# Performance work log

Measured on AMD Instinct MI355X. Metric: run time of the kernel, lower is better.

## Reference

```python
import jax, jax.numpy as jnp
import numpy as np

B, S, H, NH, FF = 16, 1024, 768, 12, 3072
D = H // NH  # 64
EPS = 1e-12


def layer_norm(x, g, b):
    mu = jnp.mean(x, axis=-1, keepdims=True)
    var = jnp.mean(jnp.square(x - mu), axis=-1, keepdims=True)
    return (x - mu) * jax.lax.rsqrt(var + EPS) * g + b


def setup_inputs() -> dict:
    key = jax.random.key(0)
    ks = jax.random.split(key, 16)
    w = lambda k, shape: (jax.random.normal(k, shape, jnp.float32) * 0.02)
    return {
        "features": jax.random.normal(ks[0], (B, S, H), jnp.float32),
        "attention_mask": jnp.zeros((B, S), jnp.float32),  # additive mask
        "wq": w(ks[1], (H, H)), "bq": jnp.zeros((H,), jnp.float32),
        "wk": w(ks[2], (H, H)), "bk": jnp.zeros((H,), jnp.float32),
        "wv": w(ks[3], (H, H)), "bv": jnp.zeros((H,), jnp.float32),
        "wo": w(ks[4], (H, H)), "bo": jnp.zeros((H,), jnp.float32),
        "ln1_g": jnp.ones((H,), jnp.float32), "ln1_b": jnp.zeros((H,), jnp.float32),
        "w1": w(ks[5], (H, FF)), "b1": jnp.zeros((FF,), jnp.float32),
        "w2": w(ks[6], (FF, H)), "b2": jnp.zeros((H,), jnp.float32),
        "ln2_g": jnp.ones((H,), jnp.float32), "ln2_b": jnp.zeros((H,), jnp.float32),
        "wp": w(ks[7], (H, H)), "bp": jnp.zeros((H,), jnp.float32),
        "wm": w(ks[8], (H, 1)), "bm": jnp.zeros((1,), jnp.float32),
    }


def reference(features, attention_mask, wq, bq, wk, bk, wv, bv, wo, bo,
              ln1_g, ln1_b, w1, b1, w2, b2, ln2_g, ln2_b, wp, bp, wm, bm):
    mask = attention_mask[:, None, None, :]  # [B,1,1,S]

    def split_heads(x):  # [B,S,H] -> [B,NH,S,D]
        return x.reshape(B, S, NH, D).transpose(0, 2, 1, 3)

    q = split_heads(features @ wq + bq)
    k = split_heads(features @ wk + bk)
    v = split_heads(features @ wv + bv)

    scores = jnp.einsum("bhqd,bhkd->bhqk", q, k) / np.sqrt(D).astype(np.float32)
    probs = jax.nn.softmax(scores + mask, axis=-1)  # dropout is identity (eval)
    ctx = jnp.einsum("bhqk,bhkd->bhqd", probs, v)
    ctx = ctx.transpose(0, 2, 1, 3).reshape(B, S, H)

    attn_out = layer_norm(ctx @ wo + bo + features, ln1_g, ln1_b)
    ffn = jax.nn.gelu(attn_out @ w1 + b1, approximate=False) @ w2 + b2
    hidden = layer_norm(ffn + attn_out, ln2_g, ln2_b)

    pooled = jnp.tanh(hidden[:, 0] @ wp + bp)  # BertPooler on [CLS]
    cls = (pooled @ wm + bm).squeeze()  # [B]
    return cls
```

## Files before the change

### kernel.cpp

```cpp
#include <hip/hip_runtime.h>
#include <math.h>

namespace {

constexpr int B  = 16;
constexpr int S  = 1024;
constexpr int H  = 768;
constexpr int NH = 12;
constexpr int DH = 64;
constexpr int FF = 3072;
constexpr int KSPL = 16;
constexpr float EPS = 1e-12f;

__device__ __forceinline__ float waveReduceSum(float v) {
#pragma unroll
    for (int d = 1; d < 64; d <<= 1) v += __shfl_xor(v, d);
    return v;
}

__device__ __forceinline__ float blockReduceSum768(float v, float* red) {
    const int lane = threadIdx.x & 63;
    const int wid  = threadIdx.x >> 6;
    v = waveReduceSum(v);
    __syncthreads();
    if (lane == 0) red[wid] = v;
    __syncthreads();
    float s = 0.f;
#pragma unroll
    for (int w = 0; w < 12; ++w) s += red[w];
    return s;
}

template <int K, int ISPL, int N>
__global__ __launch_bounds__(256) void gemm_partial(
        const float* __restrict__ A, int lda, int jtOfsA,
        const float* __restrict__ W, float* __restrict__ part) {
    constexpr int IR = K / ISPL;
    __shared__ float Asl[B * IR];
    const int jt  = blockIdx.x;
    const int sp  = blockIdx.y;
    const int i0  = sp * IR;
    const int tid = threadIdx.x;

    for (int e = tid; e < B * IR; e += 256) {
        const int b = e / IR, ii = e % IR;
        Asl[e] = A[(size_t)b * lda + (size_t)jt * jtOfsA + i0 + ii];
    }
    __syncthreads();

    const int jl = tid & 63;
    const int bg = tid >> 6;
    const int j  = jt * 64 + jl;
    const float* wp_ = W + (size_t)i0 * N + j;
    const float* a0 = Asl + (bg * 4 + 0) * IR;
    const float* a1 = Asl + (bg * 4 + 1) * IR;
    const float* a2 = Asl + (bg * 4 + 2) * IR;
    const float* a3 = Asl + (bg * 4 + 3) * IR;
    float acc0 = 0.f, acc1 = 0.f, acc2 = 0.f, acc3 = 0.f;
#pragma unroll
    for (int ii = 0; ii < IR; ++ii) {
        const float w = wp_[(size_t)ii * N];
        acc0 += w * a0[ii];
        acc1 += w * a1[ii];
        acc2 += w * a2[ii];
        acc3 += w * a3[ii];
    }
    float* pp = part + ((size_t)sp * B) * N + j;
    pp[(size_t)(bg * 4 + 0) * N] = acc0;
    pp[(size_t)(bg * 4 + 1) * N] = acc1;
    pp[(size_t)(bg * 4 + 2) * N] = acc2;
    pp[(size_t)(bg * 4 + 3) * N] = acc3;
}

template <int K, int ISPL, int N, int RED>
__global__ __launch_bounds__(256) void gemm_partial_red(
        const float* __restrict__ Ain, const float* __restrict__ bias,
        const float* __restrict__ W, float* __restrict__ part) {
    constexpr int IR = K / ISPL;
    __shared__ float Asl[B * IR];
    const int jt  = blockIdx.x;
    const int sp  = blockIdx.y;
    const int i0  = sp * IR;
    const int tid = threadIdx.x;

    for (int e = tid; e < B * IR; e += 256) {
        const int b = e / IR, ii = e % IR;
        float v = bias[i0 + ii];
#pragma unroll
        for (int sp2 = 0; sp2 < RED; ++sp2)
            v += Ain[((size_t)sp2 * B + b) * K + i0 + ii];
        Asl[e] = v;
    }
    __syncthreads();

    const int jl = tid & 63;
    const int bg = tid >> 6;
    const int j  = jt * 64 + jl;
    const float* wp_ = W + (size_t)i0 * N + j;
    const float* a0 = Asl + (bg * 4 + 0) * IR;
    const float* a1 = Asl + (bg * 4 + 1) * IR;
    const float* a2 = Asl + (bg * 4 + 2) * IR;
    const float* a3 = Asl + (bg * 4 + 3) * IR;
    float acc0 = 0.f, acc1 = 0.f, acc2 = 0.f, acc3 = 0.f;
#pragma unroll
    for (int ii = 0; ii < IR; ++ii) {
        const float w = wp_[(size_t)ii * N];
        acc0 += w * a0[ii];
        acc1 += w * a1[ii];
        acc2 += w * a2[ii];
        acc3 += w * a3[ii];
    }
    float* pp = part + ((size_t)sp * B) * N + j;
    pp[(size_t)(bg * 4 + 0) * N] = acc0;
    pp[(size_t)(bg * 4 + 1) * N] = acc1;
    pp[(size_t)(bg * 4 + 2) * N] = acc2;
    pp[(size_t)(bg * 4 + 3) * N] = acc3;
}

template <int K, int ISPL, int N, int RED>
__global__ __launch_bounds__(256) void gemm_partial_red_gelu(
        const float* __restrict__ Ain, const float* __restrict__ bias,
        const float* __restrict__ W, float* __restrict__ part) {
    constexpr int IR = K / ISPL;
    __shared__ float Asl[B * IR];
    const int jt  = blockIdx.x;
    const int sp  = blockIdx.y;
    const int i0  = sp * IR;
    const int tid = threadIdx.x;

    for (int e = tid; e < B * IR; e += 256) {
        const int b = e / IR, ii = e % IR;
        float v = bias[i0 + ii];
#pragma unroll
        for (int sp2 = 0; sp2 < RED; ++sp2)
            v += Ain[((size_t)sp2 * B + b) * K + i0 + ii];
        Asl[e] = 0.5f * v * (1.0f + erff(v * 0.70710678118654752440f));
    }
    __syncthreads();

    const int jl = tid & 63;
    const int bg = tid >> 6;
    const int j  = jt * 64 + jl;
    const float* wp_ = W + (size_t)i0 * N + j;
    const float* a0 = Asl + (bg * 4 + 0) * IR;
    const float* a1 = Asl + (bg * 4 + 1) * IR;
    const float* a2 = Asl + (bg * 4 + 2) * IR;
    const float* a3 = Asl + (bg * 4 + 3) * IR;
    float acc0 = 0.f, acc1 = 0.f, acc2 = 0.f, acc3 = 0.f;
#pragma unroll 32
    for (int ii = 0; ii < IR; ++ii) {
        const float w = wp_[(size_t)ii * N];
        acc0 += w * a0[ii];
        acc1 += w * a1[ii];
        acc2 += w * a2[ii];
        acc3 += w * a3[ii];
    }
    float* pp = part + ((size_t)sp * B) * N + j;
    pp[(size_t)(bg * 4 + 0) * N] = acc0;
    pp[(size_t)(bg * 4 + 1) * N] = acc1;
    pp[(size_t)(bg * 4 + 2) * N] = acc2;
    pp[(size_t)(bg * 4 + 3) * N] = acc3;
}

template <int ISPL>
__global__ __launch_bounds__(256) void gemm_xpart(
        const float* __restrict__ xpart, const float* __restrict__ W,
        float* __restrict__ part) {
    constexpr int IR = H / ISPL;
    __shared__ float Asl[B * IR];
    const int jt  = blockIdx.x;
    const int sp  = blockIdx.y;
    const int i0  = sp * IR;
    const int tid = threadIdx.x;

    for (int e = tid; e < B * IR; e += 256) {
        const int b = e / IR, ii = e % IR;
        float v = 0.f;
#pragma unroll
        for (int s2 = 0; s2 < KSPL; ++s2)
            v += xpart[(((size_t)(b * KSPL + s2)) * NH + jt) * H + i0 + ii];
        Asl[e] = v;
    }
    __syncthreads();

    const int jl = tid & 63;
    const int bg = tid >> 6;
    const int j  = jt * 64 + jl;
    const float* wp_ = W + (size_t)i0 * H + j;
    const float* a0 = Asl + (bg * 4 + 0) * IR;
    const float* a1 = Asl + (bg * 4 + 1) * IR;
    const float* a2 = Asl + (bg * 4 + 2) * IR;
    const float* a3 = Asl + (bg * 4 + 3) * IR;
    float acc0 = 0.f, acc1 = 0.f, acc2 = 0.f, acc3 = 0.f;
#pragma unroll
    for (int ii = 0; ii < IR; ++ii) {
        const float w = wp_[(size_t)ii * H];
        acc0 += w * a0[ii];
        acc1 += w * a1[ii];
        acc2 += w * a2[ii];
        acc3 += w * a3[ii];
    }
    float* pp = part + ((size_t)sp * B) * H + j;
    pp[(size_t)(bg * 4 + 0) * H] = acc0;
    pp[(size_t)(bg * 4 + 1) * H] = acc1;
    pp[(size_t)(bg * 4 + 2) * H] = acc2;
    pp[(size_t)(bg * 4 + 3) * H] = acc3;
}

__global__ __launch_bounds__(256) void u_kernel(
        const float* __restrict__ q0_part, const float* __restrict__ bq,
        const float* __restrict__ wk, const float* __restrict__ bk,
        float* __restrict__ u, float* __restrict__ constk) {
    const int b = blockIdx.x / NH, h = blockIdx.x % NH;
    __shared__ float qh[DH];
    const int tid = threadIdx.x;
    if (tid < DH) {
        float v = bq[h * DH + tid];
#pragma unroll
        for (int sp = 0; sp < 24; ++sp)
            v += q0_part[((size_t)sp * B + b) * H + h * DH + tid];
        qh[tid] = v;
    }
    __syncthreads();
    if (tid < DH) {
        float v = bk[h * DH + tid] * qh[tid];
        v = waveReduceSum(v);
        if (tid == 0) constk[b * NH + h] = v;
    }
    const int jj = tid & 3, iq = tid >> 2;
    const float4* qv = (const float4*)qh;
    float4 q4[4];
#pragma unroll
    for (int c = 0; c < 4; ++c) q4[c] = qv[jj * 4 + c];
#pragma unroll 4
    for (int ir = 0; ir < 12; ++ir) {
        const int i = ir * 64 + iq;
        const float4* wr = (const float4*)(wk + (size_t)i * H + h * DH);
        float s = 0.f;
#pragma unroll
        for (int c = 0; c < 4; ++c) {
            const float4 w = wr[jj * 4 + c];
            s += w.x * q4[c].x + w.y * q4[c].y + w.z * q4[c].z + w.w * q4[c].w;
        }
        s += __shfl_xor(s, 1);
        s += __shfl_xor(s, 2);
        if (jj == 0) u[((size_t)(b * NH + h)) * H + i] = s;
    }
}

__global__ __launch_bounds__(256, 2) void score_kernel(
        const float* __restrict__ x, const float* __restrict__ u,
        const float* __restrict__ constk, const float* __restrict__ mask,
        float* __restrict__ e_t, float* __restrict__ psum) {
    const int b  = blockIdx.x;
    const int kt = blockIdx.y;
    __shared__ __align__(16) float ul[NH * H];
    __shared__ float ck[NH];
    __shared__ float wsum[4][NH];
    const int tid = threadIdx.x;
    {
        const float4* ug = (const float4*)(u + (size_t)b * NH * H);
        float4* ul4 = (float4*)ul;
        for (int e = tid; e < NH * H / 4; e += 256) ul4[e] = ug[e];
        if (tid < NH) ck[tid] = constk[b * NH + tid];
    }
    __syncthreads();

    const int jj = tid & 15, kk = tid >> 4;
    const int k0 = kt * 32 + kk * 2;
    float4 xv0[12], xv1[12];
    {
        const float4* xr0 = (const float4*)(x + ((size_t)b * S + k0) * H);
        const float4* xr1 = (const float4*)(x + ((size_t)b * S + k0 + 1) * H);
#pragma unroll
        for (int t = 0; t < 12; ++t) { xv0[t] = xr0[jj + 16 * t]; xv1[t] = xr1[jj + 16 * t]; }
    }
    const float4* ul4 = (const float4*)ul;
    float acc0[NH], acc1[NH];
#pragma unroll
    for (int h = 0; h < NH; ++h) {
        float a0 = 0.f, a1 = 0.f;
#pragma unroll
        for (int t = 0; t < 12; ++t) {
            const float4 uv = ul4[h * 192 + jj + 16 * t];
            a0 += xv0[t].x * uv.x + xv0[t].y * uv.y + xv0[t].z * uv.z + xv0[t].w * uv.w;
            a1 += xv1[t].x * uv.x + xv1[t].y * uv.y + xv1[t].z * uv.z + xv1[t].w * uv.w;
        }
        acc0[h] = a0; acc1[h] = a1;
    }
#pragma unroll
    for (int h = 0; h < NH; ++h) {
#pragma unroll
        for (int d = 1; d < 16; d <<= 1) {
            acc0[h] += __shfl_xor(acc0[h], d);
            acc1[h] += __shfl_xor(acc1[h], d);
        }
    }
    const float mk0 = mask[b * S + k0];
    const float mk1 = mask[b * S + k0 + 1];
    float e0[NH], e1[NH], ps[NH];
#pragma unroll
    for (int h = 0; h < NH; ++h) {
        e0[h] = expf(acc0[h] * 0.125f + ck[h] + mk0);
        e1[h] = expf(acc1[h] * 0.125f + ck[h] + mk1);
        ps[h] = e0[h] + e1[h];
    }
    if (jj == 0) {
        float4* er0 = (float4*)(e_t + ((size_t)(b * S + k0)) * NH);
        float4* er1 = (float4*)(e_t + ((size_t)(b * S + k0 + 1)) * NH);
        er0[0] = make_float4(e0[0], e0[1], e0[2], e0[3]);
        er0[1] = make_float4(e0[4], e0[5], e0[6], e0[7]);
        er0[2] = make_float4(e0[8], e0[9], e0[10], e0[11]);
        er1[0] = make_float4(e1[0], e1[1], e1[2], e1[3]);
        er1[1] = make_float4(e1[4], e1[5], e1[6], e1[7]);
        er1[2] = make_float4(e1[8], e1[9], e1[10], e1[11]);
    }
#pragma unroll
    for (int h = 0; h < NH; ++h) {
        ps[h] += __shfl_xor(ps[h], 16);
        ps[h] += __shfl_xor(ps[h], 32);
    }
    const int wid = tid >> 6;
    if ((tid & 63) == 0) {
#pragma unroll
        for (int h = 0; h < NH; ++h) wsum[wid][h] = ps[h];
    }
    __syncthreads();
    if (tid < NH)
        psum[((size_t)(b * 32 + kt)) * NH + tid] =
            wsum[0][tid] + wsum[1][tid] + wsum[2][tid] + wsum[3][tid];
}

__global__ __launch_bounds__(768) void xbar_partial(
        const float* __restrict__ x, const float* __restrict__ e_t,
        const float* __restrict__ psum, float* __restrict__ xpart) {
    constexpr int KR = S / KSPL;
    const int b = blockIdx.x, sp = blockIdx.y;
    const int tid = threadIdx.x;
    __shared__ float rinv[NH];
    if (tid < NH) {
        float s = 0.f;
#pragma unroll
        for (int kt = 0; kt < 32; ++kt) s += psum[((size_t)(b * 32 + kt)) * NH + tid];
        rinv[tid] = 1.0f / s;
    }
    float acc[NH];
#pragma unroll
    for (int h = 0; h < NH; ++h) acc[h] = 0.f;
    const float* xr = x + ((size_t)b * S + sp * KR) * H + tid;
    const float* er = e_t + ((size_t)b * S + sp * KR) * NH;
#pragma unroll 8
    for (int kk = 0; kk < KR; ++kk) {
        const float xv = xr[(size_t)kk * H];
#pragma unroll
        for (int h = 0; h < NH; ++h) acc[h] += er[kk * NH + h] * xv;
    }
    __syncthreads();
    float* op = xpart + ((size_t)(b * KSPL + sp)) * NH * H + tid;
#pragma unroll
    for (int h = 0; h < NH; ++h) op[(size_t)h * H] = acc[h] * rinv[h];
}

template <int ISPL>
__global__ __launch_bounds__(768) void ln_kernel(
        const float* __restrict__ part, const float* __restrict__ bias,
        const float* __restrict__ resid, int residStride,
        const float* __restrict__ g, const float* __restrict__ bet,
        float* __restrict__ out) {
    __shared__ float red[12];
    const int b = blockIdx.x, j = threadIdx.x;
    float v = bias[j] + resid[(size_t)b * residStride + j];
#pragma unroll
    for (int sp = 0; sp < ISPL; ++sp) v += part[((size_t)sp * B + b) * H + j];
    const float mu = blockReduceSum768(v, red) * (1.0f / H);
    const float d  = v - mu;
    const float var = blockReduceSum768(d * d, red) * (1.0f / H);
    out[(size_t)b * H + j] = d * rsqrtf(var + EPS) * g[j] + bet[j];
}

template <int ISPL>
__global__ __launch_bounds__(768) void cls_kernel(
        const float* __restrict__ part, const float* __restrict__ bp,
        const float* __restrict__ wm, const float* __restrict__ bm,
        float* __restrict__ out) {
    __shared__ float red[12];
    const int b = blockIdx.x, j = threadIdx.x;
    float v = bp[j];
#pragma unroll
    for (int sp = 0; sp < ISPL; ++sp) v += part[((size_t)sp * B + b) * H + j];
    v = tanhf(v);
    const float s = blockReduceSum768(v * wm[j], red);
    if (j == 0) out[b] = s + bm[0];
}

}

extern "C" void kernel_launch(void* const* d_in, const int* in_sizes, int n_in,
                              void* d_out, int out_size, void* d_ws, size_t ws_size,
                              hipStream_t stream) {
    const float* x    = (const float*)d_in[0];
    const float* mask = (const float*)d_in[1];
    const float* wq   = (const float*)d_in[2];
    const float* bq   = (const float*)d_in[3];
    const float* wk   = (const float*)d_in[4];
    const float* bk   = (const float*)d_in[5];
    const float* wv   = (const float*)d_in[6];
    const float* bv   = (const float*)d_in[7];
    const float* wo   = (const float*)d_in[8];
    const float* bo   = (const float*)d_in[9];
    const float* ln1g = (const float*)d_in[10];
    const float* ln1b = (const float*)d_in[11];
    const float* w1   = (const float*)d_in[12];
    const float* b1   = (const float*)d_in[13];
    const float* w2   = (const float*)d_in[14];
    const float* b2   = (const float*)d_in[15];
    const float* ln2g = (const float*)d_in[16];
    const float* ln2b = (const float*)d_in[17];
    const float* wp   = (const float*)d_in[18];
    const float* bp   = (const float*)d_in[19];
    const float* wm   = (const float*)d_in[20];
    const float* bm   = (const float*)d_in[21];
    float* out = (float*)d_out;

    float* ws = (float*)d_ws;
    size_t o = 0;
    float* u        = ws + o; o += (size_t)B * NH * H;
    float* constk   = ws + o; o += 256;
    float* e_t      = ws + o; o += (size_t)B * S * NH;
    float* psum     = ws + o; o += (size_t)B * 32 * NH;
    float* attn_out = ws + o; o += (size_t)B * H;
    float* hidden   = ws + o; o += (size_t)B * H;
    float* arena    = ws + o;
    float* q0_part   = arena;
    float* xpart     = arena;
    float* ctx_part  = arena + (size_t)KSPL * B * NH * H;
    float* wo_part   = ctx_part + (size_t)24 * B * H;
    float* ffn1_part = arena;
    float* ffn2_part = arena + (size_t)24 * B * FF;
    float* pool_part = arena;
    (void)ws_size; (void)in_sizes; (void)n_in; (void)out_size;

    gemm_partial<H, 24, H><<<dim3(12, 24), 256, 0, stream>>>(x, S * H, 0, wq, q0_part);

    u_kernel<<<B * NH, 256, 0, stream>>>(q0_part, bq, wk, bk, u, constk);

    score_kernel<<<dim3(B, S / 32), 256, 0, stream>>>(x, u, constk, mask, e_t, psum);

    xbar_partial<<<dim3(B, KSPL), 768, 0, stream>>>(x, e_t, psum, xpart);

    gemm_xpart<24><<<dim3(12, 24), 256, 0, stream>>>(xpart, wv, ctx_part);

    gemm_partial_red<H, 24, H, 24><<<dim3(12, 24), 256, 0, stream>>>(ctx_part, bv, wo, wo_part);
    ln_kernel<24><<<B, 768, 0, stream>>>(wo_part, bo, x, S * H, ln1g, ln1b, attn_out);

    gemm_partial<H, 24, FF><<<dim3(48, 24), 256, 0, stream>>>(attn_out, H, 0, w1, ffn1_part);
    gemm_partial_red_gelu<FF, 48, H, 24><<<dim3(12, 48), 256, 0, stream>>>(ffn1_part, b1, w2, ffn2_part);
    ln_kernel<48><<<B, 768, 0, stream>>>(ffn2_part, b2, attn_out, H, ln2g, ln2b, hidden);

    gemm_partial<H, 24, H><<<dim3(12, 24), 256, 0, stream>>>(hidden, H, 0, wp, pool_part);
    cls_kernel<24><<<B, 768, 0, stream>>>(pool_part, bp, wm, bm, out);
}
```

Measured before the change: 211.2 us.

## Fuse score and context-reduction kernels; fold Q projection into u kernel

Computes the CLS query projection inside the u kernel, which removes a separate GEMM launch and its partial buffer. The exp-score kernel now keeps each tile's exponentials in shared memory and immediately forms the weighted sum of x rows, so the e_t round trip through global memory and the xbar_partial launch go away. The x tile is read while still likely in cache. Softmax normalisation moves into gemm_xpart, which reduces twice as many partials (32 instead of 16). That doubles the xpart buffer and the reduction traffic in exchange.

```diff
diff --git a/kernel.cpp b/kernel.cpp
--- a/kernel.cpp
+++ b/kernel.cpp
@@ -9,7 +9,7 @@
 constexpr int NH = 12;
 constexpr int DH = 64;
 constexpr int FF = 3072;
-constexpr int KSPL = 16;
+constexpr int XSPL = 32;
 constexpr float EPS = 1e-12f;
 
 __device__ __forceinline__ float waveReduceSum(float v) {
@@ -164,22 +164,32 @@
 
 template <int ISPL>
 __global__ __launch_bounds__(256) void gemm_xpart(
-        const float* __restrict__ xpart, const float* __restrict__ W,
-        float* __restrict__ part) {
+        const float* __restrict__ xpart, const float* __restrict__ psum,
+        const float* __restrict__ W, float* __restrict__ part) {
     constexpr int IR = H / ISPL;
     __shared__ float Asl[B * IR];
+    __shared__ float rinvl[B];
     const int jt  = blockIdx.x;
     const int sp  = blockIdx.y;
     const int i0  = sp * IR;
     const int tid = threadIdx.x;
 
+    if (tid < B) {
+        float s = 0.f;
+#pragma unroll
+        for (int kt = 0; kt < XSPL; ++kt)
+            s += psum[((size_t)(tid * XSPL + kt)) * NH + jt];
+        rinvl[tid] = 1.0f / s;
+    }
+    __syncthreads();
+
     for (int e = tid; e < B * IR; e += 256) {
-        const int b = e / IR, ii = e % IR;
+        const int bb = e / IR, ii = e % IR;
         float v = 0.f;
 #pragma unroll
-        for (int s2 = 0; s2 < KSPL; ++s2)
-            v += xpart[(((size_t)(b * KSPL + s2)) * NH + jt) * H + i0 + ii];
-        Asl[e] = v;
+        for (int s2 = 0; s2 < XSPL; ++s2)
+            v += xpart[(((size_t)(bb * XSPL + s2)) * NH + jt) * H + i0 + ii];
+        Asl[e] = v * rinvl[bb];
     }
     __syncthreads();
 
@@ -207,26 +217,36 @@
     pp[(size_t)(bg * 4 + 3) * H] = acc3;
 }
 
-__global__ __launch_bounds__(256) void u_kernel(
-        const float* __restrict__ q0_part, const float* __restrict__ bq,
-        const float* __restrict__ wk, const float* __restrict__ bk,
+__global__ __launch_bounds__(256) void qu_kernel(
+        const float* __restrict__ x, const float* __restrict__ wq,
+        const float* __restrict__ bq, const float* __restrict__ wk,
+        const float* __restrict__ bk,
         float* __restrict__ u, float* __restrict__ constk) {
     const int b = blockIdx.x / NH, h = blockIdx.x % NH;
     __shared__ float qh[DH];
-    const int tid = threadIdx.x;
-    if (tid < DH) {
-        float v = bq[h * DH + tid];
-#pragma unroll
-        for (int sp = 0; sp < 24; ++sp)
-            v += q0_part[((size_t)sp * B + b) * H + h * DH + tid];
-        qh[tid] = v;
-    }
+    __shared__ float red[4][DH];
+    const int tid = threadIdx.x;
+    const int d = tid & 63, seg = tid >> 6;
+
+    {
+        const float* xr  = x + (size_t)b * S * H;
+        const float* wqp = wq + (size_t)(seg * 192) * H + h * DH + d;
+        float acc = 0.f;
+#pragma unroll 8
+        for (int i = 0; i < 192; ++i)
+            acc += xr[seg * 192 + i] * wqp[(size_t)i * H];
+        red[seg][d] = acc;
+    }
+    __syncthreads();
+    if (tid < DH)
+        qh[tid] = bq[h * DH + tid] + red[0][tid] + red[1][tid] + red[2][tid] + red[3][tid];
     __syncthreads();
     if (tid < DH) {
         float v = bk[h * DH + tid] * qh[tid];
         v = waveReduceSum(v);
         if (tid == 0) constk[b * NH + h] = v;
     }
+
     const int jj = tid & 3, iq = tid >> 2;
     const float4* qv = (const float4*)qh;
     float4 q4[4];
@@ -248,15 +268,16 @@
     }
 }
 
-__global__ __launch_bounds__(256, 2) void score_kernel(
+__global__ __launch_bounds__(256, 2) void score_xbar_kernel(
         const float* __restrict__ x, const float* __restrict__ u,
         const float* __restrict__ constk, const float* __restrict__ mask,
-        float* __restrict__ e_t, float* __restrict__ psum) {
+        float* __restrict__ psum, float* __restrict__ xpart) {
     const int b  = blockIdx.x;
     const int kt = blockIdx.y;
     __shared__ __align__(16) float ul[NH * H];
     __shared__ float ck[NH];
     __shared__ float wsum[4][NH];
+    __shared__ __align__(16) float el[32][NH];
     const int tid = threadIdx.x;
     {
         const float4* ug = (const float4*)(u + (size_t)b * NH * H);
@@ -306,14 +327,11 @@
         ps[h] = e0[h] + e1[h];
     }
     if (jj == 0) {
-        float4* er0 = (float4*)(e_t + ((size_t)(b * S + k0)) * NH);
-        float4* er1 = (float4*)(e_t + ((size_t)(b * S + k0 + 1)) * NH);
-        er0[0] = make_float4(e0[0], e0[1], e0[2], e0[3]);
-        er0[1] = make_float4(e0[4], e0[5], e0[6], e0[7]);
-        er0[2] = make_float4(e0[8], e0[9], e0[10], e0[11]);
-        er1[0] = make_float4(e1[0], e1[1], e1[2], e1[3]);
-        er1[1] = make_float4(e1[4], e1[5], e1[6], e1[7]);
-        er1[2] = make_float4(e1[8], e1[9], e1[10], e1[11]);
+#pragma unroll
+        for (int h = 0; h < NH; ++h) {
+            el[kk * 2 + 0][h] = e0[h];
+            el[kk * 2 + 1][h] = e1[h];
+        }
     }
 #pragma unroll
     for (int h = 0; h < NH; ++h) {
@@ -327,38 +345,35 @@
     }
     __syncthreads();
     if (tid < NH)
-        psum[((size_t)(b * 32 + kt)) * NH + tid] =
+        psum[((size_t)(b * XSPL + kt)) * NH + tid] =
             wsum[0][tid] + wsum[1][tid] + wsum[2][tid] + wsum[3][tid];
-}
-
-__global__ __launch_bounds__(768) void xbar_partial(
-        const float* __restrict__ x, const float* __restrict__ e_t,
-        const float* __restrict__ psum, float* __restrict__ xpart) {
-    constexpr int KR = S / KSPL;
-    const int b = blockIdx.x, sp = blockIdx.y;
-    const int tid = threadIdx.x;
-    __shared__ float rinv[NH];
-    if (tid < NH) {
-        float s = 0.f;
-#pragma unroll
-        for (int kt = 0; kt < 32; ++kt) s += psum[((size_t)(b * 32 + kt)) * NH + tid];
-        rinv[tid] = 1.0f / s;
-    }
-    float acc[NH];
-#pragma unroll
-    for (int h = 0; h < NH; ++h) acc[h] = 0.f;
-    const float* xr = x + ((size_t)b * S + sp * KR) * H + tid;
-    const float* er = e_t + ((size_t)b * S + sp * KR) * NH;
+
+    float accx[3][NH];
+#pragma unroll
+    for (int c = 0; c < 3; ++c)
+#pragma unroll
+        for (int h = 0; h < NH; ++h) accx[c][h] = 0.f;
+    const float* xb = x + ((size_t)b * S + (size_t)kt * 32) * H;
 #pragma unroll 8
-    for (int kk = 0; kk < KR; ++kk) {
-        const float xv = xr[(size_t)kk * H];
-#pragma unroll
-        for (int h = 0; h < NH; ++h) acc[h] += er[kk * NH + h] * xv;
-    }
-    __syncthreads();
-    float* op = xpart + ((size_t)(b * KSPL + sp)) * NH * H + tid;
-#pragma unroll
-    for (int h = 0; h < NH; ++h) op[(size_t)h * H] = acc[h] * rinv[h];
+    for (int k = 0; k < 32; ++k) {
+        const float xs0 = xb[(size_t)k * H + tid];
+        const float xs1 = xb[(size_t)k * H + tid + 256];
+        const float xs2 = xb[(size_t)k * H + tid + 512];
+#pragma unroll
+        for (int h = 0; h < NH; ++h) {
+            const float ee = el[k][h];
+            accx[0][h] += ee * xs0;
+            accx[1][h] += ee * xs1;
+            accx[2][h] += ee * xs2;
+        }
+    }
+    float* op = xpart + ((size_t)(b * XSPL + kt)) * NH * H + tid;
+#pragma unroll
+    for (int h = 0; h < NH; ++h) {
+        op[(size_t)h * H +   0] = accx[0][h];
+        op[(size_t)h * H + 256] = accx[1][h];
+        op[(size_t)h * H + 512] = accx[2][h];
+    }
 }
 
 template <int ISPL>
@@ -426,29 +441,23 @@
     size_t o = 0;
     float* u        = ws + o; o += (size_t)B * NH * H;
     float* constk   = ws + o; o += 256;
-    float* e_t      = ws + o; o += (size_t)B * S * NH;
-    float* psum     = ws + o; o += (size_t)B * 32 * NH;
+    float* psum     = ws + o; o += (size_t)B * XSPL * NH;
     float* attn_out = ws + o; o += (size_t)B * H;
     float* hidden   = ws + o; o += (size_t)B * H;
     float* arena    = ws + o;
-    float* q0_part   = arena;
     float* xpart     = arena;
-    float* ctx_part  = arena + (size_t)KSPL * B * NH * H;
+    float* ctx_part  = arena + (size_t)XSPL * B * NH * H;
     float* wo_part   = ctx_part + (size_t)24 * B * H;
     float* ffn1_part = arena;
     float* ffn2_part = arena + (size_t)24 * B * FF;
     float* pool_part = arena;
     (void)ws_size; (void)in_sizes; (void)n_in; (void)out_size;
 
-    gemm_partial<H, 24, H><<<dim3(12, 24), 256, 0, stream>>>(x, S * H, 0, wq, q0_part);
-
-    u_kernel<<<B * NH, 256, 0, stream>>>(q0_part, bq, wk, bk, u, constk);
-
-    score_kernel<<<dim3(B, S / 32), 256, 0, stream>>>(x, u, constk, mask, e_t, psum);
-
-    xbar_partial<<<dim3(B, KSPL), 768, 0, stream>>>(x, e_t, psum, xpart);
-
-    gemm_xpart<24><<<dim3(12, 24), 256, 0, stream>>>(xpart, wv, ctx_part);
+    qu_kernel<<<B * NH, 256, 0, stream>>>(x, wq, bq, wk, bk, u, constk);
+
+    score_xbar_kernel<<<dim3(B, S / 32), 256, 0, stream>>>(x, u, constk, mask, psum, xpart);
+
+    gemm_xpart<24><<<dim3(12, 24), 256, 0, stream>>>(xpart, psum, wv, ctx_part);
 
     gemm_partial_red<H, 24, H, 24><<<dim3(12, 24), 256, 0, stream>>>(ctx_part, bv, wo, wo_part);
     ln_kernel<24><<<B, 768, 0, stream>>>(wo_part, bo, x, S * H, ln1g, ln1b, attn_out);
```

New measurement: 217.2 us. +2.9%, slower.
